# Optimization experiments

Hardware: AMD Instinct MI355X
Metric: run time of the kernel (lower is better)

## Reference

```python
import jax, jax.numpy as jnp
import numpy as np

B, C, H, W = 8, 256, 32, 32
N_HEAD, D_K, D_V, OUT_C = 8, 32, 32, 256


def _relative_indices(height, width):
    # idx[i, j] = (y_j - y_i + H) * W + (x_j - x_i + W), matching the torch loop
    ys, xs = np.meshgrid(np.arange(height), np.arange(width), indexing='ij')
    ys, xs = ys.reshape(-1), xs.reshape(-1)  # [L]
    rel_y = ys[None, :] - ys[:, None] + height  # [L, L]
    rel_x = xs[None, :] - xs[:, None] + width
    return jnp.asarray(rel_y * width + rel_x, dtype=jnp.int32)


def setup_inputs() -> dict:
    key = jax.random.key(0)
    ks = jax.random.split(key, 7)
    sc = lambda fan_in: 1.0 / np.sqrt(fan_in)
    table = ((2 * H - 1) * (2 * W - 1))  # 3969
    return {
        'x': jax.random.normal(ks[0], (B, C, H, W), jnp.float32),
        'Qw': jax.random.normal(ks[1], (C, N_HEAD * D_K), jnp.float32) * sc(C),
        'Kw': jax.random.normal(ks[2], (C, N_HEAD * D_K), jnp.float32) * sc(C),
        'Vw': jax.random.normal(ks[3], (C, N_HEAD * D_V), jnp.float32) * sc(C),
        'ffw': jax.random.normal(ks[4], (N_HEAD * D_V, OUT_C), jnp.float32) * sc(N_HEAD * D_V),
        'ffb': jax.random.normal(ks[5], (OUT_C,), jnp.float32) * 0.01,
        'rel_bias': jax.random.normal(ks[6], (N_HEAD, table), jnp.float32),
        'rel_idx': _relative_indices(H, W),  # [L, L] int32
    }


def reference(x, Qw, Kw, Vw, ffw, ffb, rel_bias, rel_idx):
    b, c, h_, w_ = x.shape
    L = h_ * w_
    nh = rel_bias.shape[0]
    dk = Qw.shape[1] // nh
    dv = Vw.shape[1] // nh
    xf = x.reshape(b, c, L).transpose(0, 2, 1)  # [b, L, c]
    q = (xf @ Qw).reshape(b, L, nh, dk).transpose(0, 2, 1, 3)  # [b, h, L, dk]
    k = (xf @ Kw).reshape(b, L, nh, dk).transpose(0, 2, 1, 3)
    v = (xf @ Vw).reshape(b, L, nh, dv).transpose(0, 2, 1, 3)
    bias = rel_bias[:, rel_idx]  # gather -> [h, L, L]
    sim = jnp.einsum('bhid,bhjd->bhij', q, k) + bias[None]  # no 1/sqrt(dk) in original
    attn = jax.nn.softmax(sim, axis=-1)  # dropout is identity in eval
    out = jnp.einsum('bhij,bhjd->bhid', attn, v)  # [b, h, L, dv]
    out = out.transpose(0, 2, 1, 3).reshape(b, L, nh * dv)
    out = out @ ffw + ffb  # [b, L, out_c]
    return out.transpose(0, 2, 1).reshape(b, -1, h_, w_)
```

## Files before the change

kernel.cpp:

```cpp
#include <hip/hip_runtime.h>
#include <math.h>


typedef unsigned short u16;
typedef __bf16 bf16;
typedef bf16 bf16x8 __attribute__((ext_vector_type(8)));
typedef bf16 bf16x4 __attribute__((ext_vector_type(4)));
typedef short s16x4 __attribute__((ext_vector_type(4)));
typedef float f32x4 __attribute__((ext_vector_type(4)));
typedef float f32x4u __attribute__((ext_vector_type(4), aligned(4)));
typedef u16 u16x8 __attribute__((ext_vector_type(8)));
typedef u16 u16x4 __attribute__((ext_vector_type(4)));

#define DEVI __device__ __forceinline__

DEVI u16 bfbits(float f) { return __builtin_bit_cast(u16, (bf16)f); }

DEVI void async_cp16(const u16* g, u16* l) {
    __builtin_amdgcn_global_load_lds((const __attribute__((address_space(1))) void*)g,
                                     (__attribute__((address_space(3))) void*)l, 16, 0, 0);
}

DEVI f32x4 pv_mfma(bf16x4 a, bf16x4 b, f32x4 c) {
#if __has_builtin(__builtin_amdgcn_mfma_f32_16x16x16bf16_1k)
    return __builtin_amdgcn_mfma_f32_16x16x16bf16_1k(
        __builtin_bit_cast(s16x4, a), __builtin_bit_cast(s16x4, b), c, 0, 0, 0);
#else
    asm("s_nop 1\n\tv_mfma_f32_16x16x16_bf16 %0, %1, %2, %0"
        : "+v"(c) : "v"(a), "v"(b));
    return c;
#endif
}

__global__ __launch_bounds__(256) void prep(const float* __restrict__ X,
                                            const float* __restrict__ Qw, const float* __restrict__ Kw,
                                            const float* __restrict__ Vw, const float* __restrict__ Fw,
                                            const float* __restrict__ RB,
                                            u16* __restrict__ XF, u16* __restrict__ WT,
                                            float* __restrict__ RBs) {
    __shared__ u16 t[64 * 65];
    const int blk = blockIdx.x, tid = threadIdx.x;
    if (blk < 576) {
        const float* src;
        int cbase, rbase, rows_total;
        u16* dst;
        if (blk < 512) {
            const int b = blk >> 6;
            cbase = (blk & 3) * 64; rbase = ((blk >> 2) & 15) * 64;
            src = X + (size_t)b * 256 * 1024; dst = XF + (size_t)b * 1024 * 256;
            rows_total = 1024;
        } else {
            const int t2 = blk - 512, wsel = t2 >> 4;
            cbase = (t2 & 3) * 64; rbase = ((t2 >> 2) & 3) * 64;
            src = wsel == 0 ? Qw : wsel == 1 ? Kw : wsel == 2 ? Vw : Fw;
            dst = WT + (size_t)wsel * 256 * 256;
            rows_total = 256;
        }
        const int w = tid >> 6, r = tid & 63;
#pragma unroll
        for (int i = 0; i < 16; i++) {
            const int c = w * 16 + i;
            t[c * 65 + r] = bfbits(src[(size_t)(cbase + c) * rows_total + rbase + r]);
        }
        __syncthreads();
#pragma unroll
        for (int i = 0; i < 2; i++) {
            const int idx = i * 256 + tid;
            const int r2 = idx >> 3, cg = idx & 7;
            u16x8 v;
#pragma unroll
            for (int j = 0; j < 8; j++) v[j] = t[(cg * 8 + j) * 65 + r2];
            *(u16x8*)&dst[(size_t)(rbase + r2) * 256 + cbase + cg * 8] = v;
        }
    } else {
        const int n = 8 * 3969;
        for (int i = (blk - 576) * 256 + tid; i < n; i += 32 * 256)
            RBs[i] = RB[i] * 1.44269504f;
    }
}

template <int MFR, int PASS>
__global__ __launch_bounds__(256, 3) void gemm_fused(const u16* __restrict__ xf, const u16* __restrict__ wt,
                                                     u16* __restrict__ q, u16* __restrict__ kk,
                                                     u16* __restrict__ vt, const u16* __restrict__ ob,
                                                     float* __restrict__ outf, const float* __restrict__ ffb) {
    constexpr int TM = MFR * 32;
    __shared__ __align__(16) u16 lA[2][TM * 32];
    __shared__ __align__(16) u16 lB[2][64 * 32];
    const int tid = threadIdx.x;
    const int wave = tid >> 6, lane = tid & 63;
    const int quad = lane >> 4, l15 = lane & 15;

    int mode, mbase, nbase;
    const u16 *A, *Bt;
    if (PASS == 2) {
        mode = 2; A = wt + 768 * 256; Bt = ob;
        mbase = (blockIdx.x & 3) * 64; nbase = (blockIdx.x >> 2) * 64;
    } else if (blockIdx.x < 512) {
        mode = 0; A = xf; Bt = wt;
        mbase = (blockIdx.x >> 3) * TM; nbase = (blockIdx.x & 7) * 64;
    } else {
        mode = 1; A = wt + 512 * 256; Bt = xf;
        const int t = blockIdx.x - 512;
        mbase = (t & 1) * TM; nbase = (t >> 1) * 64;
    }

    const int m0 = (wave >> 1) * (MFR * 16), n0 = (wave & 1) * 32;
    const int srow = tid >> 2;
    const int sgcol = (lane & 3) ^ ((lane >> 3) & 3);
    const int kcol = ((quad ^ ((l15 >> 1) & 3))) * 8;

    f32x4 acc[MFR][2];
#pragma unroll
    for (int i = 0; i < MFR; i++)
#pragma unroll
        for (int j = 0; j < 2; j++) acc[i][j] = f32x4{0.f, 0.f, 0.f, 0.f};

#pragma unroll
    for (int half = 0; half < MFR / 2; half++)
        async_cp16(&A[(size_t)(mbase + half * 64 + srow) * 256 + sgcol * 8],
                   &lA[0][half * 2048 + wave * 512]);
    async_cp16(&Bt[(size_t)(nbase + srow) * 256 + sgcol * 8], &lB[0][wave * 512]);
    __syncthreads();

#pragma unroll
    for (int t = 0; t < 8; ++t) {
        const int cur = t & 1;
        if (t < 7) {
            const int kb = (t + 1) * 32;
#pragma unroll
            for (int half = 0; half < MFR / 2; half++)
                async_cp16(&A[(size_t)(mbase + half * 64 + srow) * 256 + kb + sgcol * 8],
                           &lA[cur ^ 1][half * 2048 + wave * 512]);
            async_cp16(&Bt[(size_t)(nbase + srow) * 256 + kb + sgcol * 8], &lB[cur ^ 1][wave * 512]);
        }
        bf16x8 af[MFR], bfr[2];
#pragma unroll
        for (int i = 0; i < MFR; i++) af[i] = *(const bf16x8*)&lA[cur][(m0 + i * 16 + l15) * 32 + kcol];
#pragma unroll
        for (int j = 0; j < 2; j++) bfr[j] = *(const bf16x8*)&lB[cur][(n0 + j * 16 + l15) * 32 + kcol];
#pragma unroll
        for (int i = 0; i < MFR; i++)
#pragma unroll
            for (int j = 0; j < 2; j++)
                acc[i][j] = __builtin_amdgcn_mfma_f32_16x16x32_bf16(af[i], bfr[j], acc[i][j], 0, 0, 0);
        __syncthreads();
    }

#pragma unroll
    for (int i = 0; i < MFR; i++) {
#pragma unroll
        for (int j = 0; j < 2; j++) {
#pragma unroll
            for (int r = 0; r < 4; r++) {
                const int gm = mbase + m0 + i * 16 + quad * 4 + r;
                const int gn = nbase + n0 + j * 16 + l15;
                float v = acc[i][j][r];
                if (mode == 0) {
                    const int b = gm >> 10, l = gm & 1023;
                    int n = gn;
                    u16* dst = q;
                    if (n >= 256) { n -= 256; dst = kk; }
                    else v *= 1.44269504f;
                    const int h = n >> 5, d = n & 31;
                    dst[(((size_t)(b * 8 + h) * 1024 + l) << 5) + d] = bfbits(v);
                } else if (mode == 1) {
                    const int h = gm >> 5, d = gm & 31;
                    const int b = gn >> 10, l = gn & 1023;
                    vt[(((size_t)(b * 8 + h) * 32 + d) << 10) + l] = bfbits(v);
                } else {
                    const int b = gn >> 10, l = gn & 1023;
                    outf[(((size_t)(b * 256 + gm)) << 10) + l] = v + ffb[gm];
                }
            }
        }
    }
}

__global__ __launch_bounds__(256, 2) void attn(const u16* __restrict__ Q, const u16* __restrict__ Kb,
                                               const u16* __restrict__ Vt, const float* __restrict__ RBs,
                                               u16* __restrict__ O) {
    __shared__ __align__(16) u16 kbuf[4][2][32 * 32];
    __shared__ __align__(16) u16 vbuf[4][2][32 * 32];
    const int tid = threadIdx.x;
    const int wave = tid >> 6, lane = tid & 63;
    const int quad = lane >> 4, l15 = lane & 15;
    const int blk = blockIdx.x;
    const int bh = ((blk >> 6) << 3) + (blk & 7);
    const int qt = (blk >> 3) & 7;
    const int b = bh >> 3, h = bh & 7;
    const int qbase = qt * 128 + wave * 32;
    const size_t bhL = (size_t)bh * 1024;

    const bf16x8 qfA = *(const bf16x8*)&Q[(bhL + qbase + l15) * 32 + quad * 8];
    const bf16x8 qfB = *(const bf16x8*)&Q[(bhL + qbase + 16 + l15) * 32 + quad * 8];
    const float* brow0 = RBs + (size_t)h * 3969
                         + (32 - (qbase >> 5)) * 32 + 32 - l15 + quad * 4;
    const int srow = lane >> 2;
    const int sgcol = (lane & 3) ^ ((lane >> 3) & 3);
    const u16* ksrc = &Kb[bhL * 32];
    const u16* vsrc_lo = &Vt[(((size_t)bh * 32) + srow) << 10];
    const u16* vsrc_hi = &Vt[(((size_t)bh * 32) + 16 + srow) << 10];

    f32x4 oA_lo{0.f, 0.f, 0.f, 0.f}, oA_hi{0.f, 0.f, 0.f, 0.f};
    f32x4 oB_lo{0.f, 0.f, 0.f, 0.f}, oB_hi{0.f, 0.f, 0.f, 0.f};
    f32x4 sacA{0.f, 0.f, 0.f, 0.f}, sacB{0.f, 0.f, 0.f, 0.f};
    const bf16 one1 = (bf16)1.f;
    const bf16x4 onesb = {one1, one1, one1, one1};

    const int swz = (l15 >> 1) & 3;
    const int kcol = (quad ^ swz) * 8;
    const int g0 = (2 * ((quad >> 1) ^ swz) + (quad & 1)) * 4;
    const int g1 = (2 * (((quad >> 1) + 2) ^ swz) + (quad & 1)) * 4;

    f32x4u bmA, b0A, b1A, bmB, b0B, b1B;

#define BLOADA(c) do {                                          \
        bmA = *(const f32x4u*)(brow0 + (c) * 32 - 16);          \
        b0A = *(const f32x4u*)(brow0 + (c) * 32);               \
        b1A = *(const f32x4u*)(brow0 + (c) * 32 + 16);          \
    } while (0)
#define BLOADB(c) do {                                          \
        bmB = *(const f32x4u*)(brow0 + (c) * 32 - 16);          \
        b0B = *(const f32x4u*)(brow0 + (c) * 32);               \
        b1B = *(const f32x4u*)(brow0 + (c) * 32 + 16);          \
    } while (0)

#define STAGE(buf, c) do {                                                              \
        const int kb_ = (c) * 32;                                                       \
        async_cp16(ksrc + kb_ * 32 + srow * 32 + sgcol * 8, &kbuf[wave][buf][0]);       \
        async_cp16(ksrc + kb_ * 32 + 512 + srow * 32 + sgcol * 8, &kbuf[wave][buf][512]); \
        async_cp16(vsrc_lo + kb_ + sgcol * 8, &vbuf[wave][buf][0]);                     \
        async_cp16(vsrc_hi + kb_ + sgcol * 8, &vbuf[wave][buf][512]);                   \
    } while (0)

#define COMPUTE(cur, BM, B0, B1) do {                                                     \
        const bf16x8 kf0 = *(const bf16x8*)&kbuf[wave][cur][l15 * 32 + kcol];             \
        const bf16x8 kf1 = *(const bf16x8*)&kbuf[wave][cur][(16 + l15) * 32 + kcol];      \
        const bf16x4 v00 = __builtin_bit_cast(bf16x4, *(const u16x4*)&vbuf[wave][cur][l15 * 32 + g0]); \
        const bf16x4 v10 = __builtin_bit_cast(bf16x4, *(const u16x4*)&vbuf[wave][cur][l15 * 32 + g1]); \
        const bf16x4 v01 = __builtin_bit_cast(bf16x4, *(const u16x4*)&vbuf[wave][cur][(16 + l15) * 32 + g0]); \
        const bf16x4 v11 = __builtin_bit_cast(bf16x4, *(const u16x4*)&vbuf[wave][cur][(16 + l15) * 32 + g1]); \
        const f32x4 cb0 = f32x4{(B0)[0], (B0)[1], (B0)[2], (B0)[3]};                      \
        const f32x4 cb1 = f32x4{(B1)[0], (B1)[1], (B1)[2], (B1)[3]};                      \
        const f32x4 cbm = f32x4{(BM)[0], (BM)[1], (BM)[2], (BM)[3]};                      \
        f32x4 s0A = __builtin_amdgcn_mfma_f32_16x16x32_bf16(kf0, qfA, cb0, 0, 0, 0);      \
        f32x4 s1A = __builtin_amdgcn_mfma_f32_16x16x32_bf16(kf1, qfA, cb1, 0, 0, 0);      \
        f32x4 s0B = __builtin_amdgcn_mfma_f32_16x16x32_bf16(kf0, qfB, cbm, 0, 0, 0);      \
        f32x4 s1B = __builtin_amdgcn_mfma_f32_16x16x32_bf16(kf1, qfB, cb0, 0, 0, 0);      \
        bf16x4 p0A, p1A, p0B, p1B;                                                        \
        _Pragma("unroll")                                                                 \
        for (int r = 0; r < 4; r++) {                                                     \
            p0A[r] = (bf16)__builtin_amdgcn_exp2f(s0A[r]);                                \
            p1A[r] = (bf16)__builtin_amdgcn_exp2f(s1A[r]);                                \
            p0B[r] = (bf16)__builtin_amdgcn_exp2f(s0B[r]);                                \
            p1B[r] = (bf16)__builtin_amdgcn_exp2f(s1B[r]);                                \
        }                                                                                 \
        oA_lo = pv_mfma(p0A, v00, oA_lo);                                                 \
        oA_hi = pv_mfma(p0A, v01, oA_hi);                                                 \
        oA_lo = pv_mfma(p1A, v10, oA_lo);                                                 \
        oA_hi = pv_mfma(p1A, v11, oA_hi);                                                 \
        sacA = pv_mfma(p0A, onesb, sacA);                                                 \
        sacA = pv_mfma(p1A, onesb, sacA);                                                 \
        oB_lo = pv_mfma(p0B, v00, oB_lo);                                                 \
        oB_hi = pv_mfma(p0B, v01, oB_hi);                                                 \
        oB_lo = pv_mfma(p1B, v10, oB_lo);                                                 \
        oB_hi = pv_mfma(p1B, v11, oB_hi);                                                 \
        sacB = pv_mfma(p0B, onesb, sacB);                                                 \
        sacB = pv_mfma(p1B, onesb, sacB);                                                 \
    } while (0)

#define WAIT4 asm volatile("s_waitcnt vmcnt(4)" ::: "memory")
#define WAIT7 asm volatile("s_waitcnt vmcnt(7)" ::: "memory")
#define WAIT0 asm volatile("s_waitcnt vmcnt(0)" ::: "memory")
#define DSDRAIN asm volatile("s_waitcnt lgkmcnt(0)" ::: "memory")

    BLOADA(0); BLOADB(1);
    STAGE(0, 0);
    STAGE(1, 1);
    WAIT4; COMPUTE(0, bmA, b0A, b1A); DSDRAIN; BLOADA(2); STAGE(0, 2);
    WAIT7; COMPUTE(1, bmB, b0B, b1B); DSDRAIN; BLOADB(3); STAGE(1, 3);
    for (int c = 2; c < 28; c += 2) {
        WAIT7; COMPUTE(0, bmA, b0A, b1A); DSDRAIN; BLOADA(c + 2); STAGE(0, c + 2);
        WAIT7; COMPUTE(1, bmB, b0B, b1B); DSDRAIN; BLOADB(c + 3); STAGE(1, c + 3);
    }
    WAIT7; COMPUTE(0, bmA, b0A, b1A); DSDRAIN; BLOADA(30); STAGE(0, 30);
    WAIT7; COMPUTE(1, bmB, b0B, b1B); DSDRAIN; BLOADB(31); STAGE(1, 31);
    WAIT7; COMPUTE(0, bmA, b0A, b1A);
    WAIT0; COMPUTE(1, bmB, b0B, b1B);
#undef BLOADA
#undef BLOADB
#undef STAGE
#undef COMPUTE
#undef WAIT4
#undef WAIT7
#undef WAIT0
#undef DSDRAIN

#pragma unroll
    for (int r = 0; r < 4; r++) {
        const float invA = 1.f / sacA[r];
        const float invB = 1.f / sacB[r];
        const int iA = qbase + quad * 4 + r;
        const int iB = iA + 16;
        O[((size_t)(b * 1024 + iA) * 256) + h * 32 + l15] = bfbits(oA_lo[r] * invA);
        O[((size_t)(b * 1024 + iA) * 256) + h * 32 + 16 + l15] = bfbits(oA_hi[r] * invA);
        O[((size_t)(b * 1024 + iB) * 256) + h * 32 + l15] = bfbits(oB_lo[r] * invB);
        O[((size_t)(b * 1024 + iB) * 256) + h * 32 + 16 + l15] = bfbits(oB_hi[r] * invB);
    }
}

extern "C" void kernel_launch(void* const* d_in, const int* in_sizes, int n_in,
                              void* d_out, int out_size, void* d_ws, size_t ws_size,
                              hipStream_t stream) {
    const float* x   = (const float*)d_in[0];
    const float* Qw  = (const float*)d_in[1];
    const float* Kw  = (const float*)d_in[2];
    const float* Vw  = (const float*)d_in[3];
    const float* Fw  = (const float*)d_in[4];
    const float* ffb = (const float*)d_in[5];
    const float* RB  = (const float*)d_in[6];

    u16* ws = (u16*)d_ws;
    u16* xf = ws;
    u16* wt = xf + 2097152;
    u16* q  = wt + 262144;
    u16* kk = q  + 2097152;
    u16* vt = kk + 2097152;
    float* RBs = (float*)(vt + 2097152);
    u16* ob = xf;

    prep<<<dim3(608), 256, 0, stream>>>(x, Qw, Kw, Vw, Fw, RB, xf, wt, RBs);
    gemm_fused<4, 0><<<dim3(768), 256, 0, stream>>>(xf, wt, q, kk, vt, nullptr, nullptr, nullptr);
    attn<<<dim3(512), 256, 0, stream>>>(q, kk, vt, RBs, ob);
    gemm_fused<2, 2><<<dim3(512), 256, 0, stream>>>(xf, wt, q, kk, vt, ob, (float*)d_out, ffb);
}
```

Baseline: 116.7 us.

## Share K/V LDS tiles across waves with barrier-synchronized double buffering

Before this change, each of the four waves staged its own private copy of the same K/V chunk into LDS. Now one shared double-buffered K/V tile serves the whole block: each wave issues one quarter of the async loads, and block barriers replace the per-wave waits and LDS drains. This cuts redundant global loads and LDS footprint by four times, which may allow higher occupancy. In exchange it adds a block-wide barrier per chunk that couples the waves. It also passes the bias into the MFMA accumulator by bit-cast instead of rebuilding the vectors element by element.

```diff
diff --git a/kernel.cpp b/kernel.cpp
--- a/kernel.cpp
+++ b/kernel.cpp
@@ -180,8 +180,8 @@
 __global__ __launch_bounds__(256, 2) void attn(const u16* __restrict__ Q, const u16* __restrict__ Kb,
                                                const u16* __restrict__ Vt, const float* __restrict__ RBs,
                                                u16* __restrict__ O) {
-    __shared__ __align__(16) u16 kbuf[4][2][32 * 32];
-    __shared__ __align__(16) u16 vbuf[4][2][32 * 32];
+    __shared__ __align__(16) u16 kbuf[2][32 * 32];
+    __shared__ __align__(16) u16 vbuf[2][32 * 32];
     const int tid = threadIdx.x;
     const int wave = tid >> 6, lane = tid & 63;
     const int quad = lane >> 4, l15 = lane & 15;
@@ -226,28 +226,29 @@
         b1B = *(const f32x4u*)(brow0 + (c) * 32 + 16);          \
     } while (0)
 
-#define STAGE(buf, c) do {                                                              \
-        const int kb_ = (c) * 32;                                                       \
-        async_cp16(ksrc + kb_ * 32 + srow * 32 + sgcol * 8, &kbuf[wave][buf][0]);       \
-        async_cp16(ksrc + kb_ * 32 + 512 + srow * 32 + sgcol * 8, &kbuf[wave][buf][512]); \
-        async_cp16(vsrc_lo + kb_ + sgcol * 8, &vbuf[wave][buf][0]);                     \
-        async_cp16(vsrc_hi + kb_ + sgcol * 8, &vbuf[wave][buf][512]);                   \
+#define STAGE(buf, c) do {                                                                   \
+        const int kb_ = (c) * 32;                                                            \
+        if (wave == 0)                                                                       \
+            async_cp16(ksrc + kb_ * 32 + srow * 32 + sgcol * 8, &kbuf[buf][0]);              \
+        else if (wave == 1)                                                                  \
+            async_cp16(ksrc + kb_ * 32 + 512 + srow * 32 + sgcol * 8, &kbuf[buf][512]);      \
+        else if (wave == 2)                                                                  \
+            async_cp16(vsrc_lo + kb_ + sgcol * 8, &vbuf[buf][0]);                            \
+        else                                                                                 \
+            async_cp16(vsrc_hi + kb_ + sgcol * 8, &vbuf[buf][512]);                          \
     } while (0)
 
 #define COMPUTE(cur, BM, B0, B1) do {                                                     \
-        const bf16x8 kf0 = *(const bf16x8*)&kbuf[wave][cur][l15 * 32 + kcol];             \
-        const bf16x8 kf1 = *(const bf16x8*)&kbuf[wave][cur][(16 + l15) * 32 + kcol];      \
-        const bf16x4 v00 = __builtin_bit_cast(bf16x4, *(const u16x4*)&vbuf[wave][cur][l15 * 32 + g0]); \
-        const bf16x4 v10 = __builtin_bit_cast(bf16x4, *(const u16x4*)&vbuf[wave][cur][l15 * 32 + g1]); \
-        const bf16x4 v01 = __builtin_bit_cast(bf16x4, *(const u16x4*)&vbuf[wave][cur][(16 + l15) * 32 + g0]); \
-        const bf16x4 v11 = __builtin_bit_cast(bf16x4, *(const u16x4*)&vbuf[wave][cur][(16 + l15) * 32 + g1]); \
-        const f32x4 cb0 = f32x4{(B0)[0], (B0)[1], (B0)[2], (B0)[3]};                      \
-        const f32x4 cb1 = f32x4{(B1)[0], (B1)[1], (B1)[2], (B1)[3]};                      \
-        const f32x4 cbm = f32x4{(BM)[0], (BM)[1], (BM)[2], (BM)[3]};                      \
-        f32x4 s0A = __builtin_amdgcn_mfma_f32_16x16x32_bf16(kf0, qfA, cb0, 0, 0, 0);      \
-        f32x4 s1A = __builtin_amdgcn_mfma_f32_16x16x32_bf16(kf1, qfA, cb1, 0, 0, 0);      \
-        f32x4 s0B = __builtin_amdgcn_mfma_f32_16x16x32_bf16(kf0, qfB, cbm, 0, 0, 0);      \
-        f32x4 s1B = __builtin_amdgcn_mfma_f32_16x16x32_bf16(kf1, qfB, cb0, 0, 0, 0);      \
+        const bf16x8 kf0 = *(const bf16x8*)&kbuf[cur][l15 * 32 + kcol];                   \
+        const bf16x8 kf1 = *(const bf16x8*)&kbuf[cur][(16 + l15) * 32 + kcol];            \
+        const bf16x4 v00 = __builtin_bit_cast(bf16x4, *(const u16x4*)&vbuf[cur][l15 * 32 + g0]); \
+        const bf16x4 v10 = __builtin_bit_cast(bf16x4, *(const u16x4*)&vbuf[cur][l15 * 32 + g1]); \
+        const bf16x4 v01 = __builtin_bit_cast(bf16x4, *(const u16x4*)&vbuf[cur][(16 + l15) * 32 + g0]); \
+        const bf16x4 v11 = __builtin_bit_cast(bf16x4, *(const u16x4*)&vbuf[cur][(16 + l15) * 32 + g1]); \
+        f32x4 s0A = __builtin_amdgcn_mfma_f32_16x16x32_bf16(kf0, qfA, __builtin_bit_cast(f32x4, (B0)), 0, 0, 0); \
+        f32x4 s1A = __builtin_amdgcn_mfma_f32_16x16x32_bf16(kf1, qfA, __builtin_bit_cast(f32x4, (B1)), 0, 0, 0); \
+        f32x4 s0B = __builtin_amdgcn_mfma_f32_16x16x32_bf16(kf0, qfB, __builtin_bit_cast(f32x4, (BM)), 0, 0, 0); \
+        f32x4 s1B = __builtin_amdgcn_mfma_f32_16x16x32_bf16(kf1, qfB, __builtin_bit_cast(f32x4, (B0)), 0, 0, 0); \
         bf16x4 p0A, p1A, p0B, p1B;                                                        \
         _Pragma("unroll")                                                                 \
         for (int r = 0; r < 4; r++) {                                                     \
@@ -270,32 +271,26 @@
         sacB = pv_mfma(p1B, onesb, sacB);                                                 \
     } while (0)
 
-#define WAIT4 asm volatile("s_waitcnt vmcnt(4)" ::: "memory")
-#define WAIT7 asm volatile("s_waitcnt vmcnt(7)" ::: "memory")
+#define WAIT3 asm volatile("s_waitcnt vmcnt(3)" ::: "memory")
 #define WAIT0 asm volatile("s_waitcnt vmcnt(0)" ::: "memory")
-#define DSDRAIN asm volatile("s_waitcnt lgkmcnt(0)" ::: "memory")
+#define BAR __builtin_amdgcn_s_barrier()
 
     BLOADA(0); BLOADB(1);
     STAGE(0, 0);
-    STAGE(1, 1);
-    WAIT4; COMPUTE(0, bmA, b0A, b1A); DSDRAIN; BLOADA(2); STAGE(0, 2);
-    WAIT7; COMPUTE(1, bmB, b0B, b1B); DSDRAIN; BLOADB(3); STAGE(1, 3);
-    for (int c = 2; c < 28; c += 2) {
-        WAIT7; COMPUTE(0, bmA, b0A, b1A); DSDRAIN; BLOADA(c + 2); STAGE(0, c + 2);
-        WAIT7; COMPUTE(1, bmB, b0B, b1B); DSDRAIN; BLOADB(c + 3); STAGE(1, c + 3);
-    }
-    WAIT7; COMPUTE(0, bmA, b0A, b1A); DSDRAIN; BLOADA(30); STAGE(0, 30);
-    WAIT7; COMPUTE(1, bmB, b0B, b1B); DSDRAIN; BLOADB(31); STAGE(1, 31);
-    WAIT7; COMPUTE(0, bmA, b0A, b1A);
-    WAIT0; COMPUTE(1, bmB, b0B, b1B);
+    WAIT0; BAR;
+    for (int c = 0; c < 30; c += 2) {
+        STAGE(1, c + 1); COMPUTE(0, bmA, b0A, b1A); BLOADA(c + 2); WAIT3; BAR;
+        STAGE(0, c + 2); COMPUTE(1, bmB, b0B, b1B); BLOADB(c + 3); WAIT3; BAR;
+    }
+    STAGE(1, 31); COMPUTE(0, bmA, b0A, b1A); WAIT0; BAR;
+    COMPUTE(1, bmB, b0B, b1B);
 #undef BLOADA
 #undef BLOADB
 #undef STAGE
 #undef COMPUTE
-#undef WAIT4
-#undef WAIT7
+#undef WAIT3
 #undef WAIT0
-#undef DSDRAIN
+#undef BAR
 
 #pragma unroll
     for (int r = 0; r < 4; r++) {
```

After: 120.8 us. +3.5%, slower.
